# Performance work log

Hardware: AMD Instinct MI355X
Metric: run time of the kernel (lower is better)

Reference implementation:

```python
import jax, jax.numpy as jnp
import numpy as np

B, S, D = 2, 2048, 2048
HQ, HKV, HD = 16, 4, 128
G = HQ // HKV  # repeat factor for GQA
SCALE = HD ** -0.5


def setup_inputs() -> dict:
    key = jax.random.key(0)
    k = jax.random.split(key, 6)
    return {
        "x": jax.random.normal(k[0], (B, S, D), jnp.float32),
        "Wq": jax.random.normal(k[1], (D, HQ * HD), jnp.float32) * 0.02,
        "Wk": jax.random.normal(k[2], (D, HKV * HD), jnp.float32) * 0.02,
        "Wv": jax.random.normal(k[3], (D, HKV * HD), jnp.float32) * 0.02,
        "Wo": jax.random.normal(k[4], (HQ * HD, D), jnp.float32) * 0.02,
        "bo": jnp.zeros((D,), jnp.float32),
    }


def reference(x, Wq, Wk, Wv, Wo, bo):
    b, s, _ = x.shape
    # projections (Linear, no bias for q/k/v)
    q = (x @ Wq).reshape(b, s, HQ, HD).transpose(0, 2, 1, 3)    # [b,Hq,s,hd]
    k = (x @ Wk).reshape(b, s, HKV, HD).transpose(0, 2, 1, 3)   # [b,Hkv,s,hd]
    v = (x @ Wv).reshape(b, s, HKV, HD).transpose(0, 2, 1, 3)
    # group query heads per kv head: repeat_interleave(k, G, dim=1) means
    # q head h attends to kv head h // G -> reshape q to [b,Hkv,G,s,hd]
    qg = q.reshape(b, HKV, G, s, HD)
    sim = jnp.einsum("bkgid,bkjd->bkgij", qg, k) * SCALE        # [b,Hkv,G,s,s]
    attn = jax.nn.softmax(sim, axis=-1)                          # dropout p=0 (eval)
    out = jnp.einsum("bkgij,bkjd->bkgid", attn, v)               # [b,Hkv,G,s,hd]
    out = out.reshape(b, HQ, s, HD).transpose(0, 2, 1, 3).reshape(b, s, HQ * HD)
    return out @ Wo + bo
```

## Files before the change

### kernel.cpp

```cpp
#include <hip/hip_runtime.h>
#include <hip/hip_bf16.h>
#include <stdint.h>

typedef unsigned short u16;
typedef __attribute__((ext_vector_type(8))) short short8;
typedef __attribute__((ext_vector_type(4))) float f32x4;

#define B_N   2
#define S_LEN 2048
#define D_MOD 2048
#define N_HQ  16
#define N_HKV 4
#define N_HD  128

__device__ __forceinline__ u16 f2b(float f) {
  union { float f; uint32_t u; } v; v.f = f;
  uint32_t r = v.u + 0x7fffu + ((v.u >> 16) & 1u);
  return (u16)(r >> 16);
}

__device__ __forceinline__ uint32_t pack2_rhu(float a, float b) {
  union { float f; uint32_t u; } va, vb;
  va.f = a; vb.f = b;
  return __builtin_amdgcn_perm(vb.u + 0x8000u, va.u + 0x8000u, 0x07060302u);
}

__device__ __forceinline__ void gload_lds16(const void* g, void* l) {
  __builtin_amdgcn_global_load_lds((__attribute__((address_space(1))) void*)g,
                                   (__attribute__((address_space(3))) void*)l,
                                   16, 0, 0);
}

__global__ void k_pre(const float* __restrict__ x, u16* __restrict__ x_bf,
                      const float* __restrict__ Wq, const float* __restrict__ Wk,
                      const float* __restrict__ Wv, const float* __restrict__ Wo,
                      u16* __restrict__ Wqt, u16* __restrict__ Wkt,
                      u16* __restrict__ Wvt, u16* __restrict__ Wot) {
  const int bid = blockIdx.x;
  if (bid < 4096) {
    int i = (bid * 256 + threadIdx.x) * 8;
    float4 a = *(const float4*)(x + i);
    float4 b = *(const float4*)(x + i + 4);
    short8 o;
    o[0] = (short)f2b(a.x); o[1] = (short)f2b(a.y);
    o[2] = (short)f2b(a.z); o[3] = (short)f2b(a.w);
    o[4] = (short)f2b(b.x); o[5] = (short)f2b(b.y);
    o[6] = (short)f2b(b.z); o[7] = (short)f2b(b.w);
    *(short8*)(x_bf + i) = o;
    return;
  }
  __shared__ float tile[32][33];
  const int idx = bid - 4096;
  const int cb = idx % 160;
  const int k0 = (idx / 160) * 32;
  const float* W; u16* Wt; int N, n0;
  if (cb < 64)      { W = Wq; Wt = Wqt; N = 2048; n0 = cb * 32; }
  else if (cb < 80) { W = Wk; Wt = Wkt; N = 512;  n0 = (cb - 64) * 32; }
  else if (cb < 96) { W = Wv; Wt = Wvt; N = 512;  n0 = (cb - 80) * 32; }
  else              { W = Wo; Wt = Wot; N = 2048; n0 = (cb - 96) * 32; }
  const int tx = threadIdx.x & 31, ty = threadIdx.x >> 5;
#pragma unroll
  for (int i = 0; i < 4; i++) {
    int r = ty + i * 8;
    tile[r][tx] = W[(size_t)(k0 + r) * N + n0 + tx];
  }
  __syncthreads();
#pragma unroll
  for (int i = 0; i < 4; i++) {
    int r = ty + i * 8;
    Wt[(size_t)(n0 + r) * 2048 + k0 + tx] = f2b(tile[tx][r]);
  }
}

__global__ __launch_bounds__(256, 3) void k_gemm_qkv(
    const u16* __restrict__ A,
    const u16* __restrict__ Wqt, const u16* __restrict__ Wkt, const u16* __restrict__ Wvt,
    u16* __restrict__ Qout, u16* __restrict__ Kout, u16* __restrict__ Vt,
    float qscale)
{
  __shared__ __attribute__((aligned(16))) u16 lA[128 * 64];
  __shared__ __attribute__((aligned(16))) u16 lB[128 * 64];
  const int K = D_MOD;
  const int tid = threadIdx.x;
  const int lane = tid & 63, w = tid >> 6;
  const int wr = w >> 1, wc = w & 1;
  const int lin = blockIdx.y * 24 + blockIdx.x;
  const int swz = (lin & 7) * 96 + (lin >> 3);
  const int bx = swz % 24;
  const int kind = bx < 16 ? 0 : (bx < 20 ? 1 : 2);
  const int bcol = (kind == 0 ? bx : (bx & 3)) * 128;
  const u16* Bt = kind == 0 ? Wqt : (kind == 1 ? Wkt : Wvt);
  const int brow = (swz / 24) * 128;
  const int lrow = lane >> 3;
  const int l15 = lane & 15, lg = lane >> 4;
  const int l7a = l15 & 7;

  f32x4 acc[4][4] = {};

  for (int kt = 0; kt < K; kt += 64) {
#pragma unroll
    for (int i = 0; i < 4; i++) {
      int row = (w * 4 + i) * 8 + lrow;
      int ch = (lane & 7) ^ (row & 7);
      gload_lds16(A + (size_t)(brow + row) * K + kt + ch * 8, &lA[(w * 4 + i) * 512]);
      gload_lds16(Bt + (size_t)(bcol + row) * K + kt + ch * 8, &lB[(w * 4 + i) * 512]);
    }
    __syncthreads();
#pragma unroll
    for (int kk = 0; kk < 2; kk++) {
      short8 af[4], bf[4];
#pragma unroll
      for (int m = 0; m < 4; m++)
        af[m] = *(const short8*)&lA[(wr * 64 + m * 16 + l15) * 64 + (((kk * 4 + lg) ^ l7a) * 8)];
#pragma unroll
      for (int n = 0; n < 4; n++)
        bf[n] = *(const short8*)&lB[(wc * 64 + n * 16 + l15) * 64 + (((kk * 4 + lg) ^ l7a) * 8)];
#pragma unroll
      for (int m = 0; m < 4; m++)
#pragma unroll
        for (int n = 0; n < 4; n++)
          acc[m][n] = __builtin_amdgcn_mfma_f32_16x16x32_bf16(af[m], bf[n], acc[m][n], 0, 0, 0);
    }
    __syncthreads();
  }

#pragma unroll
  for (int m = 0; m < 4; m++) {
#pragma unroll
    for (int n = 0; n < 4; n++) {
#pragma unroll
      for (int r = 0; r < 4; r++) {
        float v = acc[m][n][r];
        int row = brow + wr * 64 + m * 16 + lg * 4 + r;
        int col = bcol + wc * 64 + n * 16 + l15;
        if (kind == 0) {
          Qout[(size_t)row * (N_HQ * N_HD) + col] = f2b(v * qscale);
        } else if (kind == 1) {
          Kout[(size_t)row * (N_HKV * N_HD) + col] = f2b(v);
        } else {
          int bb = row >> 11, s = row & 2047;
          int hkv = col >> 7, d = col & 127;
          Vt[((size_t)((bb * N_HKV + hkv) * N_HD + d)) * S_LEN + s] = f2b(v);
        }
      }
    }
  }
}

__global__ __launch_bounds__(256, 3) void k_gemm_o(
    const u16* __restrict__ A, const u16* __restrict__ Bt,
    float* __restrict__ Cout, const float* __restrict__ bias,
    int M, int N, int K)
{
  __shared__ __attribute__((aligned(16))) u16 lA[128 * 64];
  __shared__ __attribute__((aligned(16))) u16 lB[128 * 64];
  const int tid = threadIdx.x;
  const int lane = tid & 63, w = tid >> 6;
  const int wr = w >> 1, wc = w & 1;
  const int lin = blockIdx.y * 16 + blockIdx.x;
  const int swz = (lin & 7) * 64 + (lin >> 3);
  const int brow = (swz / 16) * 128, bcol = (swz % 16) * 128;
  const int lrow = lane >> 3;
  const int l15 = lane & 15, lg = lane >> 4;
  const int l7a = l15 & 7;

  f32x4 acc[4][4] = {};

  for (int kt = 0; kt < K; kt += 64) {
#pragma unroll
    for (int i = 0; i < 4; i++) {
      int row = (w * 4 + i) * 8 + lrow;
      int ch = (lane & 7) ^ (row & 7);
      gload_lds16(A + (size_t)(brow + row) * K + kt + ch * 8, &lA[(w * 4 + i) * 512]);
      gload_lds16(Bt + (size_t)(bcol + row) * K + kt + ch * 8, &lB[(w * 4 + i) * 512]);
    }
    __syncthreads();
#pragma unroll
    for (int kk = 0; kk < 2; kk++) {
      short8 af[4], bf[4];
#pragma unroll
      for (int m = 0; m < 4; m++)
        af[m] = *(const short8*)&lA[(wr * 64 + m * 16 + l15) * 64 + (((kk * 4 + lg) ^ l7a) * 8)];
#pragma unroll
      for (int n = 0; n < 4; n++)
        bf[n] = *(const short8*)&lB[(wc * 64 + n * 16 + l15) * 64 + (((kk * 4 + lg) ^ l7a) * 8)];
#pragma unroll
      for (int m = 0; m < 4; m++)
#pragma unroll
        for (int n = 0; n < 4; n++)
          acc[m][n] = __builtin_amdgcn_mfma_f32_16x16x32_bf16(af[m], bf[n], acc[m][n], 0, 0, 0);
    }
    __syncthreads();
  }

#pragma unroll
  for (int m = 0; m < 4; m++) {
#pragma unroll
    for (int n = 0; n < 4; n++) {
#pragma unroll
      for (int r = 0; r < 4; r++) {
        int row = brow + wr * 64 + m * 16 + lg * 4 + r;
        int col = bcol + wc * 64 + n * 16 + l15;
        Cout[(size_t)row * N + col] = acc[m][n][r] + bias[col];
      }
    }
  }
}

__global__ __launch_bounds__(256, 2) void k_attn(
    const u16* __restrict__ Q,
    const u16* __restrict__ Kb,
    const u16* __restrict__ Vt,
    u16* __restrict__ O)
{
  __shared__ __attribute__((aligned(16))) u16 lK[2][64 * 128];
  __shared__ __attribute__((aligned(16))) u16 lV[2][128 * 64];
  const int lane = threadIdx.x & 63, w = threadIdx.x >> 6;
  const int lin = blockIdx.z * 256 + blockIdx.y * 16 + blockIdx.x;
  const int swz = (lin & 7) * 64 + (lin >> 3);
  const int qt = swz & 15, h = (swz >> 4) & 15, b = swz >> 8;
  const int hkv = h >> 2;
  const int qbase = qt * 128 + w * 32;
  const int l15 = lane & 15, lg = lane >> 4;
  const int l7 = lane & 7, l3 = lane >> 3;

  const u16* kbp = Kb + (size_t)(b * S_LEN) * (N_HKV * N_HD) + hkv * N_HD;
  const u16* vbp = Vt + (size_t)((b * N_HKV + hkv) * N_HD) * S_LEN;

  short8 qf[2][4];
#pragma unroll
  for (int s = 0; s < 2; s++) {
    const u16* qptr = Q + (size_t)(b * S_LEN + qbase + s * 16 + l15) * (N_HQ * N_HD) + h * N_HD + lg * 8;
#pragma unroll
    for (int kk = 0; kk < 4; kk++) qf[s][kk] = *(const short8*)(qptr + kk * 32);
  }

  f32x4 acc_o[2][8] = {};
  f32x4 acc_ls[2] = {};
  short8 vone;
#pragma unroll
  for (int j = 0; j < 8; j++) vone[j] = (short)0x3F80;

#define STAGE(bufi, ktv) do {                                                        \
    _Pragma("unroll")                                                                \
    for (int i = 0; i < 4; i++) {                                                    \
      int kr = i * 16 + w * 4 + lg;                                                  \
      int sx = (kr & 3) ^ (((kr >> 3) & 3) << 1);                                    \
      gload_lds16(kbp + (size_t)((ktv) + kr) * (N_HKV * N_HD) + ((l15 ^ sx)) * 8,    \
                  &lK[bufi][(i * 16 + w * 4) * 128]);                                \
      int vr = i * 32 + w * 8 + l3;                                                  \
      gload_lds16(vbp + (size_t)vr * S_LEN + (ktv) + ((l7 ^ (vr & 7))) * 8,          \
                  &lV[bufi][(i * 32 + w * 8) * 64]);                                 \
    } } while (0)

  STAGE(0, 0);
  __syncthreads();

  const int sxr = (l15 & 3) ^ (((l15 >> 2) & 3) << 1);
  const int NT = S_LEN / 64;
  int buf = 0;
  for (int it = 0; it < NT; ++it) {
    if (it + 1 < NT) STAGE(buf ^ 1, (it + 1) * 64);

    f32x4 sc[2][4] = {};
    __builtin_amdgcn_s_setprio(1);
#pragma unroll
    for (int nf = 0; nf < 4; nf++) {
      int krow = (nf >> 1) * 32 + ((l15 >> 2) * 8) + ((nf & 1) * 4) + (l15 & 3);
      const u16* kro = &lK[buf][krow * 128];
#pragma unroll
      for (int kk = 0; kk < 4; kk++) {
        short8 kf = *(const short8*)&kro[(((kk * 4 + lg) ^ sxr) * 8)];
#pragma unroll
        for (int s = 0; s < 2; s++)
          sc[s][nf] = __builtin_amdgcn_mfma_f32_16x16x32_bf16(kf, qf[s][kk], sc[s][nf], 0, 0, 0);
      }
    }
    __builtin_amdgcn_s_setprio(0);

    short8 pf[2][2];
#pragma unroll
    for (int s = 0; s < 2; s++)
#pragma unroll
      for (int p2 = 0; p2 < 2; p2++) {
        union { short8 s8; uint32_t w4[4]; } u;
#pragma unroll
        for (int j = 0; j < 4; j++) {
          float lo = __builtin_amdgcn_exp2f(sc[s][p2 * 2 + (j >> 1)][(j & 1) * 2]);
          float hi = __builtin_amdgcn_exp2f(sc[s][p2 * 2 + (j >> 1)][(j & 1) * 2 + 1]);
          u.w4[j] = pack2_rhu(lo, hi);
        }
        pf[s][p2] = u.s8;
      }

    __builtin_amdgcn_s_setprio(1);
#pragma unroll
    for (int s = 0; s < 2; s++)
#pragma unroll
      for (int p2 = 0; p2 < 2; p2++)
        acc_ls[s] = __builtin_amdgcn_mfma_f32_16x16x32_bf16(pf[s][p2], vone, acc_ls[s], 0, 0, 0);

#pragma unroll
    for (int nc = 0; nc < 8; nc++) {
      int vrow = nc * 16 + l15;
      const u16* vro = &lV[buf][vrow * 64];
#pragma unroll
      for (int p2 = 0; p2 < 2; p2++) {
        short8 vf = *(const short8*)&vro[(((p2 * 4 + lg) ^ (vrow & 7)) * 8)];
#pragma unroll
        for (int s = 0; s < 2; s++)
          acc_o[s][nc] = __builtin_amdgcn_mfma_f32_16x16x32_bf16(pf[s][p2], vf, acc_o[s][nc], 0, 0, 0);
      }
    }
    __builtin_amdgcn_s_setprio(0);

    __syncthreads();
    buf ^= 1;
  }
#undef STAGE

#pragma unroll
  for (int s = 0; s < 2; s++)
#pragma unroll
    for (int r = 0; r < 4; r++) {
      float inv = 1.f / acc_ls[s][r];
      size_t row = (size_t)(b * S_LEN + qbase + s * 16 + lg * 4 + r);
#pragma unroll
      for (int nc = 0; nc < 8; nc++)
        O[row * (N_HQ * N_HD) + h * N_HD + nc * 16 + l15] = f2b(acc_o[s][nc][r] * inv);
    }
}

extern "C" void kernel_launch(void* const* d_in, const int* in_sizes, int n_in,
                              void* d_out, int out_size, void* d_ws, size_t ws_size,
                              hipStream_t stream) {
  const float* x  = (const float*)d_in[0];
  const float* Wq = (const float*)d_in[1];
  const float* Wk = (const float*)d_in[2];
  const float* Wv = (const float*)d_in[3];
  const float* Wo = (const float*)d_in[4];
  const float* bo = (const float*)d_in[5];
  float* out = (float*)d_out;

  char* ws = (char*)d_ws;
  u16* x_bf = (u16*)(ws + 0);
  u16* Wqt  = (u16*)(ws + 16777216);
  u16* Wkt  = (u16*)(ws + 25165824);
  u16* Wvt  = (u16*)(ws + 27262976);
  u16* Wot  = (u16*)(ws + 29360128);
  u16* Qb   = (u16*)(ws + 37748736);
  u16* Kbuf = (u16*)(ws + 54525952);
  u16* Vt   = (u16*)(ws + 58720256);
  u16* AO   = (u16*)(ws + 0);

  k_pre<<<14336, 256, 0, stream>>>(x, x_bf, Wq, Wk, Wv, Wo, Wqt, Wkt, Wvt, Wot);

  const float qscale = 1.4426950408889634f / sqrtf((float)N_HD);

  k_gemm_qkv<<<dim3(24, 32), 256, 0, stream>>>(
      x_bf, Wqt, Wkt, Wvt, Qb, Kbuf, Vt, qscale);

  k_attn<<<dim3(S_LEN / 128, N_HQ, B_N), 256, 0, stream>>>(Qb, Kbuf, Vt, AO);

  k_gemm_o<<<dim3(16, 32), 256, 0, stream>>>(
      AO, Wot, out, bo, B_N * S_LEN, D_MOD, N_HQ * N_HD);
}
```

Before: 180.6 us.

## Stage attention K/V tiles through registers with single LDS buffer for higher occupancy

Replaces the double-buffered direct global-to-LDS K/V loads with register prefetch of the next tile and a write into a single shared buffer after compute. This halves the attention kernel's LDS use and raises launch bounds to 4 blocks per CU so more waves can hide latency. In exchange it adds a second barrier per iteration, extra VGPR pressure from the prefetch registers, and a register-to-LDS write step that is no longer overlapped with the MFMA work.

```diff
diff --git a/kernel.cpp b/kernel.cpp
--- a/kernel.cpp
+++ b/kernel.cpp
@@ -207,14 +207,14 @@
   }
 }
 
-__global__ __launch_bounds__(256, 2) void k_attn(
+__global__ __launch_bounds__(256, 4) void k_attn(
     const u16* __restrict__ Q,
     const u16* __restrict__ Kb,
     const u16* __restrict__ Vt,
     u16* __restrict__ O)
 {
-  __shared__ __attribute__((aligned(16))) u16 lK[2][64 * 128];
-  __shared__ __attribute__((aligned(16))) u16 lV[2][128 * 64];
+  __shared__ __attribute__((aligned(16))) u16 lK[64 * 128];
+  __shared__ __attribute__((aligned(16))) u16 lV[128 * 64];
   const int lane = threadIdx.x & 63, w = threadIdx.x >> 6;
   const int lin = blockIdx.z * 256 + blockIdx.y * 16 + blockIdx.x;
   const int swz = (lin & 7) * 64 + (lin >> 3);
@@ -241,33 +241,40 @@
 #pragma unroll
   for (int j = 0; j < 8; j++) vone[j] = (short)0x3F80;
 
-#define STAGE(bufi, ktv) do {                                                        \
+  short8 kreg[4], vreg[4];
+
+#define LOADREGS(ktv) do {                                                           \
     _Pragma("unroll")                                                                \
     for (int i = 0; i < 4; i++) {                                                    \
       int kr = i * 16 + w * 4 + lg;                                                  \
       int sx = (kr & 3) ^ (((kr >> 3) & 3) << 1);                                    \
-      gload_lds16(kbp + (size_t)((ktv) + kr) * (N_HKV * N_HD) + ((l15 ^ sx)) * 8,    \
-                  &lK[bufi][(i * 16 + w * 4) * 128]);                                \
+      kreg[i] = *(const short8*)(kbp + (size_t)((ktv) + kr) * (N_HKV * N_HD) + (l15 ^ sx) * 8); \
       int vr = i * 32 + w * 8 + l3;                                                  \
-      gload_lds16(vbp + (size_t)vr * S_LEN + (ktv) + ((l7 ^ (vr & 7))) * 8,          \
-                  &lV[bufi][(i * 32 + w * 8) * 64]);                                 \
+      vreg[i] = *(const short8*)(vbp + (size_t)vr * S_LEN + (ktv) + (l7 ^ (vr & 7)) * 8);       \
     } } while (0)
 
-  STAGE(0, 0);
+#define WRITEREGS() do {                                                             \
+    _Pragma("unroll")                                                                \
+    for (int i = 0; i < 4; i++) {                                                    \
+      *(short8*)&lK[(i * 16 + w * 4) * 128 + lane * 8] = kreg[i];                    \
+      *(short8*)&lV[(i * 32 + w * 8) * 64 + lane * 8] = vreg[i];                     \
+    } } while (0)
+
+  LOADREGS(0);
+  WRITEREGS();
   __syncthreads();
 
   const int sxr = (l15 & 3) ^ (((l15 >> 2) & 3) << 1);
   const int NT = S_LEN / 64;
-  int buf = 0;
   for (int it = 0; it < NT; ++it) {
-    if (it + 1 < NT) STAGE(buf ^ 1, (it + 1) * 64);
+    if (it + 1 < NT) LOADREGS((it + 1) * 64);
 
     f32x4 sc[2][4] = {};
     __builtin_amdgcn_s_setprio(1);
 #pragma unroll
     for (int nf = 0; nf < 4; nf++) {
       int krow = (nf >> 1) * 32 + ((l15 >> 2) * 8) + ((nf & 1) * 4) + (l15 & 3);
-      const u16* kro = &lK[buf][krow * 128];
+      const u16* kro = &lK[krow * 128];
 #pragma unroll
       for (int kk = 0; kk < 4; kk++) {
         short8 kf = *(const short8*)&kro[(((kk * 4 + lg) ^ sxr) * 8)];
@@ -303,7 +310,7 @@
 #pragma unroll
     for (int nc = 0; nc < 8; nc++) {
       int vrow = nc * 16 + l15;
-      const u16* vro = &lV[buf][vrow * 64];
+      const u16* vro = &lV[vrow * 64];
 #pragma unroll
       for (int p2 = 0; p2 < 2; p2++) {
         short8 vf = *(const short8*)&vro[(((p2 * 4 + lg) ^ (vrow & 7)) * 8)];
@@ -315,9 +322,11 @@
     __builtin_amdgcn_s_setprio(0);
 
     __syncthreads();
-    buf ^= 1;
-  }
-#undef STAGE
+    if (it + 1 < NT) WRITEREGS();
+    __syncthreads();
+  }
+#undef LOADREGS
+#undef WRITEREGS
 
 #pragma unroll
   for (int s = 0; s < 2; s++)
```

New measurement: 452.7 us. +150.6%, slower.
